# Kernel tuning notes

Measured on AMD Instinct MI355X. Metric: run time of the kernel, lower is better.

The kernel has to match this reference:

```python
import jax, jax.numpy as jnp
import numpy as np

B, S, H = 2, 2048, 4096
N_HEADS, N_KV_HEADS, HEAD_DIM = 32, 8, 128
WINDOW = 1024
ROPE_THETA = 10000.0


def rotate_half(x):
    x1, x2 = jnp.split(x, 2, axis=-1)
    return jnp.concatenate((-x2, x1), axis=-1)


def rope_cache(seq_len, head_dim, theta):
    inv_freq = 1.0 / (theta ** (jnp.arange(0, head_dim, 2, dtype=jnp.float32) / head_dim))
    t = jnp.arange(seq_len, dtype=jnp.float32)
    freqs = jnp.outer(t, inv_freq)                      # [S, hd/2]
    emb = jnp.concatenate((freqs, freqs), axis=-1)      # [S, hd]
    return jnp.cos(emb), jnp.sin(emb)


def setup_inputs() -> dict:
    key = jax.random.key(0)
    k0, k1, k2, k3, k4 = jax.random.split(key, 5)
    sc_in = 1.0 / np.sqrt(H)
    return {
        "hidden_states": jax.random.normal(k0, (B, S, H), dtype=jnp.float32),
        "Wq": jax.random.normal(k1, (N_HEADS * HEAD_DIM, H), dtype=jnp.float32) * sc_in,
        "Wk": jax.random.normal(k2, (N_KV_HEADS * HEAD_DIM, H), dtype=jnp.float32) * sc_in,
        "Wv": jax.random.normal(k3, (N_KV_HEADS * HEAD_DIM, H), dtype=jnp.float32) * sc_in,
        "Wo": jax.random.normal(k4, (H, N_HEADS * HEAD_DIM), dtype=jnp.float32) * sc_in,
        "position_ids": jnp.tile(jnp.arange(S, dtype=jnp.int64 if jax.config.jax_enable_x64 else jnp.int32), (B, 1)),
    }


def reference(hidden_states, Wq, Wk, Wv, Wo, position_ids):
    b, s, h = hidden_states.shape
    n_rep = N_HEADS // N_KV_HEADS

    # projections (Linear with no bias: x @ W.T)
    q = (hidden_states @ Wq.T).reshape(b, s, N_HEADS, HEAD_DIM).transpose(0, 2, 1, 3)
    k = (hidden_states @ Wk.T).reshape(b, s, N_KV_HEADS, HEAD_DIM).transpose(0, 2, 1, 3)
    v = (hidden_states @ Wv.T).reshape(b, s, N_KV_HEADS, HEAD_DIM).transpose(0, 2, 1, 3)

    # RoPE
    cos_c, sin_c = rope_cache(s, HEAD_DIM, ROPE_THETA)
    cos = cos_c[position_ids][:, None]  # [b,1,s,hd]
    sin = sin_c[position_ids][:, None]
    q = q * cos + rotate_half(q) * sin
    k = k * cos + rotate_half(k) * sin

    # GQA repeat_kv
    k = jnp.repeat(k, n_rep, axis=1)  # [b, n_heads, s, hd]
    v = jnp.repeat(v, n_rep, axis=1)

    # sliding-window causal attention
    scores = jnp.einsum('bhqd,bhkd->bhqk', q, k) / jnp.sqrt(jnp.asarray(HEAD_DIM, q.dtype))
    i = jnp.arange(s)[:, None]
    j = jnp.arange(s)[None, :]
    allowed = (j <= i) & ((i - j) < WINDOW)  # causal + sliding window
    scores = jnp.where(allowed, scores, jnp.finfo(scores.dtype).min)
    attn = jax.nn.softmax(scores.astype(jnp.float32), axis=-1).astype(q.dtype)

    out = jnp.einsum('bhqk,bhkd->bhqd', attn, v)  # [b,h,s,hd]
    out = out.transpose(0, 2, 1, 3).reshape(b, s, N_HEADS * HEAD_DIM)
    return out @ Wo.T
```

## Files before the change

kernel.cpp:

```cpp
#include <hip/hip_runtime.h>
#include <hip/hip_bf16.h>
#include <cmath>

typedef unsigned short u16;
typedef __attribute__((ext_vector_type(8))) short bf16x8;
typedef __attribute__((ext_vector_type(4))) float f32x4;
typedef __attribute__((ext_vector_type(16))) float f32x16;
typedef __attribute__((ext_vector_type(2))) int i32x2;
typedef __attribute__((ext_vector_type(4))) unsigned int u32x4;

#define B_    2
#define S_    2048
#define H_    4096
#define NH_   32
#define NKV_  8
#define HD_   128
#define WIN_  1024

__device__ __forceinline__ u16 f2b(float f) {
  union { float f; unsigned u; } v; v.f = f;
  unsigned r = v.u + 0x7fffu + ((v.u >> 16) & 1u);
  return (u16)(r >> 16);
}
__device__ __forceinline__ float b2f(u16 h) {
  union { unsigned u; float f; } v; v.u = ((unsigned)h) << 16;
  return v.f;
}

__device__ __forceinline__ void storeC(float* p, float v) { *p = v; }
__device__ __forceinline__ void storeC(u16* p, float v)   { *p = f2b(v); }

__device__ __forceinline__ void gl2lds(const u16* g, u16* l) {
  __builtin_amdgcn_global_load_lds(
      (const __attribute__((address_space(1))) unsigned int*)(g),
      (__attribute__((address_space(3))) unsigned int*)(l), 16, 0, 0);
}

__device__ __forceinline__ i32x2 plswap(int a, int b) {
  return __builtin_amdgcn_permlane32_swap(a, b, false, false);
}
__device__ __forceinline__ unsigned pkbf16(float lo, float hi) {
  unsigned r;
  asm("v_cvt_pk_bf16_f32 %0, %1, %2" : "=v"(r) : "v"(lo), "v"(hi));
  return r;
}

__global__ __launch_bounds__(256) void cvt_bf16(const float* __restrict__ s,
                                                u16* __restrict__ d, int n4) {
  int i = blockIdx.x * 256 + threadIdx.x;
  if (i < n4) {
    float4 v = ((const float4*)s)[i];
    ushort4 o;
    o.x = f2b(v.x); o.y = f2b(v.y); o.z = f2b(v.z); o.w = f2b(v.w);
    ((ushort4*)d)[i] = o;
  }
}

template <int BM, typename OutT>
__global__ __launch_bounds__(256) void gemm_bt(const u16* __restrict__ A,
                                               const u16* __restrict__ W,
                                               OutT* __restrict__ C,
                                               int M, int N, int K) {
  __shared__ u16 As[BM * 32];
  __shared__ u16 Bs[128 * 32];
  const int t = threadIdx.x;
  const int lane = t & 63, wave = t >> 6;
  const int quad = lane >> 4, l16 = lane & 15;
  const int wm = wave >> 1, wn = wave & 1;
  constexpr int WM = BM / 2;
  constexpr int MI = WM / 16;
  const size_t m0 = (size_t)blockIdx.y * BM, n0 = (size_t)blockIdx.x * 128;

  f32x4 acc[MI][4] = {};
  const int srow = lane >> 2, skc = lane & 3;

  for (int k0 = 0; k0 < K; k0 += 32) {
    __syncthreads();
#pragma unroll
    for (int i = 0; i < BM / 64; i++) {
      int row = wave * (BM / 4) + i * 16 + srow;
      gl2lds(A + (m0 + row) * K + k0 + skc * 8, &As[row * 32 + skc * 8]);
    }
#pragma unroll
    for (int i = 0; i < 2; i++) {
      int row = wave * 32 + i * 16 + srow;
      gl2lds(W + (n0 + row) * K + k0 + skc * 8, &Bs[row * 32 + skc * 8]);
    }
    __syncthreads();
    bf16x8 af[MI], bfr[4];
#pragma unroll
    for (int i = 0; i < MI; i++)
      af[i] = *(const bf16x8*)(&As[(wm * WM + i * 16 + l16) * 32 + quad * 8]);
#pragma unroll
    for (int i = 0; i < 4; i++)
      bfr[i] = *(const bf16x8*)(&Bs[(wn * 64 + i * 16 + l16) * 32 + quad * 8]);
#pragma unroll
    for (int mi = 0; mi < MI; mi++)
#pragma unroll
      for (int nj = 0; nj < 4; nj++)
        acc[mi][nj] = __builtin_amdgcn_mfma_f32_16x16x32_bf16(
            af[mi], bfr[nj], acc[mi][nj], 0, 0, 0);
  }

#pragma unroll
  for (int mi = 0; mi < MI; mi++) {
    size_t rbase = m0 + wm * WM + mi * 16 + quad * 4;
#pragma unroll
    for (int nj = 0; nj < 4; nj++) {
      size_t col = n0 + wn * 64 + nj * 16 + l16;
#pragma unroll
      for (int e = 0; e < 4; e++)
        storeC(&C[(rbase + e) * N + col], acc[mi][nj][e]);
    }
  }
}

__global__ __launch_bounds__(256) void rope_k(u16* __restrict__ X,
                                              const int* __restrict__ pos,
                                              int log2nh) {
  int idx = blockIdx.x * 256 + threadIdx.x;
  int i = idx & 63;
  int bsh = idx >> 6;
  int h = bsh & ((1 << log2nh) - 1);
  int bs = bsh >> log2nh;
  int p = pos[bs];
  float inv = exp2f(-(float)i * (13.287712379549449f / 64.0f));
  float ang = (float)p * inv;
  float sn, c;
  sincosf(ang, &sn, &c);
  size_t base = ((((size_t)bs) << log2nh) + h) * HD_;
  float x1 = b2f(X[base + i]), x2 = b2f(X[base + i + 64]);
  X[base + i]      = f2b(x1 * c - x2 * sn);
  X[base + i + 64] = f2b(x2 * c + x1 * sn);
}

__global__ __launch_bounds__(256) void transpose_v(const u16* __restrict__ V,
                                                   u16* __restrict__ Vt) {
  __shared__ u16 tile[64][72];
  int s0 = blockIdx.x * 64, d0 = blockIdx.y * 64, bh = blockIdx.z;
  int b = bh >> 3, hk = bh & 7;
  int t = threadIdx.x;
  int r = t >> 3, c = t & 7;
#pragma unroll
  for (int i = 0; i < 2; i++) {
    int row = r + i * 32;
    uint4 v = *(const uint4*)(V + (((size_t)(b * S_ + s0 + row)) * NKV_ + hk) * HD_ + d0 + c * 8);
    *(uint4*)(&tile[row][c * 8]) = v;
  }
  __syncthreads();
#pragma unroll
  for (int i = 0; i < 2; i++) {
    int d = r + i * 32;
    u16 tmp[8];
#pragma unroll
    for (int j = 0; j < 8; j++) tmp[j] = tile[c * 8 + j][d];
    *(uint4*)(Vt + ((size_t)bh * HD_ + d0 + d) * S_ + s0 + c * 8) = *(uint4*)tmp;
  }
}

__global__ __launch_bounds__(256, 2) void attn_k(const u16* __restrict__ Q,
                                                 const u16* __restrict__ K,
                                                 const u16* __restrict__ Vt,
                                                 u16* __restrict__ O) {
  __shared__ __align__(16) u16 smem[32768];
  const int t = threadIdx.x, wave = t >> 6, lane = t & 63;
  const int cq = lane & 31, hi = lane >> 5;
  const int q0 = blockIdx.x * 128, h = blockIdx.y, b = blockIdx.z;
  const int hk = h >> 2;
  const int qw = q0 + wave * 32;
  const int q = qw + cq;
  const float SCL2 = 0.08838834764831845f * 1.4426950408889634f;

  bf16x8 qf[8];
  {
    const u16* qp = Q + ((size_t)(b * S_ + q) * NH_ + h) * HD_ + hi * 8;
#pragma unroll
    for (int c = 0; c < 8; c++) qf[c] = *(const bf16x8*)(qp + c * 16);
  }

  f32x16 oacc[4] = {};
  float m_i = -1e30f, l_i = 0.0f;

  const int rK = wave * 16 + (lane >> 4), jKl = lane & 15;
  const int rV = wave * 32 + (lane >> 3), jVl = lane & 7;
  const size_t kbase0 = (size_t)b * S_ * (NKV_ * HD_) + (size_t)hk * HD_;
  const size_t vbase0 = (size_t)(b * NKV_ + hk) * HD_ * S_;

  auto stage = [&](int bsel, int kt) {
    u16* kd = smem + bsel * 8192 + wave * 2048 + lane * 8;
    u16* vd = smem + 16384 + bsel * 8192 + wave * 2048 + lane * 8;
#pragma unroll
    for (int ii = 0; ii < 4; ii++) {
      int row = rK + 4 * ii;
      gl2lds(K + kbase0 + (size_t)(kt + row) * (NKV_ * HD_) + (jKl ^ (row & 7)) * 8,
             kd + ii * 512);
    }
#pragma unroll
    for (int ii = 0; ii < 4; ii++) {
      int row = rV + 8 * ii;
      gl2lds(Vt + vbase0 + (size_t)row * S_ + kt + (jVl ^ (row & 7)) * 8,
             vd + ii * 512);
    }
  };

  int lo = q0 - (WIN_ - 1); if (lo < 0) lo = 0;
  const int lo_t = lo & ~63;
  const int kt_max = q0 + 64;

  stage(0, lo_t);
  __syncthreads();
  int buf = 0;
  for (int kt = lo_t; kt <= kt_max; kt += 64) {
    if (kt + 64 <= kt_max) stage(buf ^ 1, kt + 64);
    if (kt <= qw + 31 && kt + 63 >= qw - (WIN_ - 1)) {
      const u16* ks = smem + buf * 8192;
      const u16* vs = smem + 16384 + buf * 8192;
      const int rx = cq & 7;
      f32x16 cs0 = {}, cs1 = {};
      __builtin_amdgcn_s_setprio(1);
#pragma unroll
      for (int c = 0; c < 8; c++) {
        const int blk = 2 * c + hi;
        bf16x8 a0 = *(const bf16x8*)(ks + cq * 128 + ((blk ^ rx) * 8));
        bf16x8 a1 = *(const bf16x8*)(ks + (32 + cq) * 128 + ((blk ^ rx) * 8));
        cs0 = __builtin_amdgcn_mfma_f32_32x32x16_bf16(a0, qf[c], cs0, 0, 0, 0);
        cs1 = __builtin_amdgcn_mfma_f32_32x32x16_bf16(a1, qf[c], cs1, 0, 0, 0);
      }
      __builtin_amdgcn_s_setprio(0);

      float sv[32];
      const bool full = (kt >= qw - 992) && (kt + 63 <= qw);
      if (full) {
#pragma unroll
        for (int r = 0; r < 16; r++) {
          sv[r] = cs0[r] * SCL2;
          sv[16 + r] = cs1[r] * SCL2;
        }
      } else {
#pragma unroll
        for (int g = 0; g < 2; g++)
#pragma unroll
          for (int r = 0; r < 16; r++) {
            int kk = kt + g * 32 + (r & 3) + 8 * (r >> 2) + 4 * hi;
            float s = (g ? cs1[r] : cs0[r]) * SCL2;
            sv[g * 16 + r] = (kk <= q && q - kk < WIN_) ? s : -1e30f;
          }
      }

      float m4[4] = {sv[0], sv[1], sv[2], sv[3]};
#pragma unroll
      for (int i = 4; i < 32; i++) m4[i & 3] = fmaxf(m4[i & 3], sv[i]);
      float mx = fmaxf(fmaxf(m4[0], m4[1]), fmaxf(m4[2], m4[3]));
      {
        i32x2 r2 = plswap(__float_as_int(mx), __float_as_int(mx));
        mx = fmaxf(__int_as_float(r2.x), __int_as_float(r2.y));
      }
      if (__any(mx > m_i + 8.0f)) {
        float mn = fmaxf(m_i, mx);
        float al = exp2f(m_i - mn);
        m_i = mn; l_i *= al;
#pragma unroll
        for (int dg = 0; dg < 4; dg++)
#pragma unroll
          for (int e = 0; e < 16; e++) oacc[dg][e] *= al;
      }
      float p[32], a4[4] = {0.f, 0.f, 0.f, 0.f};
#pragma unroll
      for (int i = 0; i < 32; i++) {
        p[i] = exp2f(sv[i] - m_i);
        a4[i & 3] += p[i];
      }
      float rs = (a4[0] + a4[1]) + (a4[2] + a4[3]);
      {
        i32x2 r2 = plswap(__float_as_int(rs), __float_as_int(rs));
        rs = __int_as_float(r2.x) + __int_as_float(r2.y);
      }
      l_i += rs;

      bf16x8 pb[4];
#pragma unroll
      for (int cc = 0; cc < 4; cc++) {
        const int bse = cc * 8;
        unsigned x0 = pkbf16(p[bse + 0], p[bse + 1]);
        unsigned y0 = pkbf16(p[bse + 4], p[bse + 5]);
        unsigned x1 = pkbf16(p[bse + 2], p[bse + 3]);
        unsigned y1 = pkbf16(p[bse + 6], p[bse + 7]);
        i32x2 w02 = plswap((int)x0, (int)y0);
        i32x2 w13 = plswap((int)x1, (int)y1);
        u32x4 wv;
        wv.x = (unsigned)w02.x; wv.y = (unsigned)w13.x;
        wv.z = (unsigned)w02.y; wv.w = (unsigned)w13.y;
        pb[cc] = __builtin_bit_cast(bf16x8, wv);
      }

      __builtin_amdgcn_s_setprio(1);
#pragma unroll
      for (int dg = 0; dg < 4; dg++) {
        const int rr = dg * 32 + cq;
#pragma unroll
        for (int cc = 0; cc < 4; cc++) {
          bf16x8 va = *(const bf16x8*)(vs + rr * 64 + (((2 * cc + hi) ^ (rr & 7)) * 8));
          oacc[dg] = __builtin_amdgcn_mfma_f32_32x32x16_bf16(va, pb[cc], oacc[dg], 0, 0, 0);
        }
      }
      __builtin_amdgcn_s_setprio(0);
    }
    __syncthreads();
    buf ^= 1;
  }

  const float inv = 1.0f / l_i;
  u16* os = smem + wave * 4352;
#pragma unroll
  for (int dg = 0; dg < 4; dg++)
#pragma unroll
    for (int e = 0; e < 16; e += 2) {
      int d = dg * 32 + (e & 3) + 8 * (e >> 2) + 4 * hi;
      unsigned pk2 = (unsigned)f2b(oacc[dg][e] * inv) |
                     ((unsigned)f2b(oacc[dg][e + 1] * inv) << 16);
      *(unsigned*)(os + cq * 136 + d) = pk2;
    }
  asm volatile("s_waitcnt lgkmcnt(0)" ::: "memory");
  __builtin_amdgcn_sched_barrier(0);
#pragma unroll
  for (int ps = 0; ps < 8; ps++) {
    int row = (lane >> 4) + ps * 4, j = lane & 15;
    uint4 vv = *(const uint4*)(os + row * 136 + j * 8);
    *(uint4*)(O + ((size_t)(b * S_ + q0 + wave * 32 + row) * NH_ + h) * HD_ + j * 8) = vv;
  }
}

extern "C" void kernel_launch(void* const* d_in, const int* in_sizes, int n_in,
                              void* d_out, int out_size, void* d_ws, size_t ws_size,
                              hipStream_t stream) {
  const float* x  = (const float*)d_in[0];
  const float* Wq = (const float*)d_in[1];
  const float* Wk = (const float*)d_in[2];
  const float* Wv = (const float*)d_in[3];
  const float* Wo = (const float*)d_in[4];
  const int*  pos = (const int*)d_in[5];
  float* out = (float*)d_out;

  const size_t BS = (size_t)B_ * S_;
  const size_t MB = 1024 * 1024;
  char* p = (char*)d_ws;
  u16* xb  = (u16*)(p);
  u16* W32 = (u16*)(p + 32 * MB);
  u16* W8  = (u16*)(p + 64 * MB);
  u16* Qb  = (u16*)(p + 72 * MB);
  u16* Kb  = (u16*)(p + 104 * MB);
  u16* Vb  = (u16*)(p + 112 * MB);
  u16* WoB = xb;
  u16* Ob  = W32;
  u16* Vt  = W8;

  auto cvt = [&](const float* src, u16* dst, size_t n) {
    int n4 = (int)(n / 4);
    cvt_bf16<<<dim3((n4 + 255) / 256), dim3(256), 0, stream>>>(src, dst, n4);
  };

  cvt(x, xb, BS * H_);
  cvt(Wq, W32, (size_t)H_ * H_);
  gemm_bt<128, u16><<<dim3(H_ / 128, BS / 128), dim3(256), 0, stream>>>(
      xb, W32, Qb, (int)BS, H_, H_);
  cvt(Wk, W8, (size_t)NKV_ * HD_ * H_);
  gemm_bt<64, u16><<<dim3(NKV_ * HD_ / 128, BS / 64), dim3(256), 0, stream>>>(
      xb, W8, Kb, (int)BS, NKV_ * HD_, H_);
  cvt(Wv, W8, (size_t)NKV_ * HD_ * H_);
  gemm_bt<64, u16><<<dim3(NKV_ * HD_ / 128, BS / 64), dim3(256), 0, stream>>>(
      xb, W8, Vb, (int)BS, NKV_ * HD_, H_);

  rope_k<<<dim3((int)(BS * NH_ * 64 / 256)), dim3(256), 0, stream>>>(Qb, pos, 5);
  rope_k<<<dim3((int)(BS * NKV_ * 64 / 256)), dim3(256), 0, stream>>>(Kb, pos, 3);

  transpose_v<<<dim3(S_ / 64, HD_ / 64, B_ * NKV_), dim3(256), 0, stream>>>(Vb, Vt);

  attn_k<<<dim3(S_ / 128, NH_, B_), dim3(256), 0, stream>>>(Qb, Kb, Vt, Ob);

  cvt(Wo, WoB, (size_t)H_ * H_);
  gemm_bt<128, float><<<dim3(H_ / 128, BS / 128), dim3(256), 0, stream>>>(
      Ob, WoB, out, (int)BS, H_, H_);
}
```

Measured before the change: 891.1 us.

## Add 256x256-tile double-buffered GEMM for Q and output projections

Adds a new GEMM kernel that uses 256x256 output tiles with 512 threads, a K-step of 64, and double-buffered LDS staging through direct global-to-LDS loads. LDS addresses are XOR-swizzled to avoid bank conflicts, workgroups are remapped so neighbours share L2 data, and MFMA priority is raised around the math. The Q and O projections now use it. The aim is to raise arithmetic intensity and overlap loads with compute on the two large 4096x4096 GEMMs, at the cost of one workgroup per CU from the 128KB LDS footprint and only 256 workgroups.

```diff
diff --git a/kernel.cpp b/kernel.cpp
--- a/kernel.cpp
+++ b/kernel.cpp
@@ -105,6 +105,93 @@
 #pragma unroll
   for (int mi = 0; mi < MI; mi++) {
     size_t rbase = m0 + wm * WM + mi * 16 + quad * 4;
+#pragma unroll
+    for (int nj = 0; nj < 4; nj++) {
+      size_t col = n0 + wn * 64 + nj * 16 + l16;
+#pragma unroll
+      for (int e = 0; e < 4; e++)
+        storeC(&C[(rbase + e) * N + col], acc[mi][nj][e]);
+    }
+  }
+}
+
+template <typename OutT>
+__global__ __launch_bounds__(512, 1) void gemm256(const u16* __restrict__ A,
+                                                  const u16* __restrict__ W,
+                                                  OutT* __restrict__ C,
+                                                  int M, int N, int K) {
+  __shared__ __align__(16) u16 smem[65536];
+  const int t = threadIdx.x;
+  const int lane = t & 63, wave = t >> 6;
+  const int quad = lane >> 4, l16 = lane & 15;
+  const int wm = wave >> 2, wn = wave & 3;
+
+  const int wg = blockIdx.x;
+  const int swz = (wg & 7) * ((int)gridDim.x >> 3) + (wg >> 3);
+  const int nbn = N >> 8;
+  const size_t m0 = (size_t)(swz / nbn) * 256, n0 = (size_t)(swz % nbn) * 256;
+
+  f32x4 acc[8][4] = {};
+
+  const int srow0 = wave * 32;
+  const int sr = lane >> 3, sj = lane & 7;
+
+  auto stage = [&](int bsel, int kt) {
+    u16* ab = smem + bsel * 16384;
+    u16* bb = smem + 32768 + bsel * 16384;
+#pragma unroll
+    for (int ii = 0; ii < 4; ii++) {
+      int row = srow0 + ii * 8 + sr;
+      int gb = (sj ^ (row & 7)) * 8;
+      gl2lds(A + (m0 + row) * K + kt + gb, ab + (srow0 + ii * 8) * 64 + lane * 8);
+      gl2lds(W + (n0 + row) * K + kt + gb, bb + (srow0 + ii * 8) * 64 + lane * 8);
+    }
+  };
+
+  stage(0, 0);
+  __syncthreads();
+  int buf = 0;
+  for (int kt = 0; kt < K; kt += 64) {
+    if (kt + 64 < K) stage(buf ^ 1, kt + 64);
+    const u16* ab = smem + buf * 16384;
+    const u16* bb = smem + 32768 + buf * 16384;
+
+    bf16x8 bfr[4][2];
+#pragma unroll
+    for (int nj = 0; nj < 4; nj++) {
+      int row = wn * 64 + nj * 16 + l16;
+#pragma unroll
+      for (int ks = 0; ks < 2; ks++)
+        bfr[nj][ks] = *(const bf16x8*)(bb + row * 64 + (((ks * 4 + quad) ^ (row & 7)) * 8));
+    }
+#pragma unroll
+    for (int p = 0; p < 4; p++) {
+      bf16x8 af[2][2];
+#pragma unroll
+      for (int mm = 0; mm < 2; mm++) {
+        int row = wm * 128 + (p * 2 + mm) * 16 + l16;
+#pragma unroll
+        for (int ks = 0; ks < 2; ks++)
+          af[mm][ks] = *(const bf16x8*)(ab + row * 64 + (((ks * 4 + quad) ^ (row & 7)) * 8));
+      }
+      __builtin_amdgcn_s_setprio(1);
+#pragma unroll
+      for (int mm = 0; mm < 2; mm++)
+#pragma unroll
+        for (int nj = 0; nj < 4; nj++)
+#pragma unroll
+          for (int ks = 0; ks < 2; ks++)
+            acc[p * 2 + mm][nj] = __builtin_amdgcn_mfma_f32_16x16x32_bf16(
+                af[mm][ks], bfr[nj][ks], acc[p * 2 + mm][nj], 0, 0, 0);
+      __builtin_amdgcn_s_setprio(0);
+    }
+    __syncthreads();
+    buf ^= 1;
+  }
+
+#pragma unroll
+  for (int mi = 0; mi < 8; mi++) {
+    size_t rbase = m0 + wm * 128 + mi * 16 + quad * 4;
 #pragma unroll
     for (int nj = 0; nj < 4; nj++) {
       size_t col = n0 + wn * 64 + nj * 16 + l16;
@@ -361,8 +448,7 @@
 
   cvt(x, xb, BS * H_);
   cvt(Wq, W32, (size_t)H_ * H_);
-  gemm_bt<128, u16><<<dim3(H_ / 128, BS / 128), dim3(256), 0, stream>>>(
-      xb, W32, Qb, (int)BS, H_, H_);
+  gemm256<u16><<<dim3(256), dim3(512), 0, stream>>>(xb, W32, Qb, (int)BS, H_, H_);
   cvt(Wk, W8, (size_t)NKV_ * HD_ * H_);
   gemm_bt<64, u16><<<dim3(NKV_ * HD_ / 128, BS / 64), dim3(256), 0, stream>>>(
       xb, W8, Kb, (int)BS, NKV_ * HD_, H_);
@@ -378,6 +464,5 @@
   attn_k<<<dim3(S_ / 128, NH_, B_), dim3(256), 0, stream>>>(Qb, Kb, Vt, Ob);
 
   cvt(Wo, WoB, (size_t)H_ * H_);
-  gemm_bt<128, float><<<dim3(H_ / 128, BS / 128), dim3(256), 0, stream>>>(
-      Ob, WoB, out, (int)BS, H_, H_);
-}
+  gemm256<float><<<dim3(256), dim3(512), 0, stream>>>(Ob, WoB, out, (int)BS, H_, H_);
+}
```

Result: faster. 766.5 us (-14.0%).
